# Kernel tuning notes

Hardware: AMD Instinct MI355X
Metric: run time of the kernel (lower is better)

## Reference

```python
import jax, jax.numpy as jnp
import numpy as np

N = 100000   # nodes (users+objects merged into one table)
M = 32768    # interactions (edges)
D = 256      # emb_dim == inter_dim
E = 2        # etypes: trusts, rates


def setup_inputs() -> dict:
    key = jax.random.key(0)
    ks = jax.random.split(key, 24)
    s = 1.0 / np.sqrt(D)
    f = lambda k, shp: (jax.random.normal(k, shp, dtype=jnp.float32) * s)
    return {
        "src": jax.random.randint(ks[0], (M,), 0, N),
        "dst": jax.random.randint(ks[1], (M,), 0, N),
        "etype": jax.random.randint(ks[2], (M,), 0, E),
        "dt": jax.random.uniform(ks[3], (M,), dtype=jnp.float32),
        "hid": f(ks[4], (N, D)),
        "cell": f(ks[5], (N, D)),
        # per-etype relation MLPs (source side and target side), layer==1 -> Lin-ReLU-Lin
        "W1s": f(ks[6], (E, D, D)), "b1s": f(ks[7], (E, D)),
        "W2s": f(ks[8], (E, D, D)), "b2s": f(ks[9], (E, D)),
        "W1g": f(ks[10], (E, D, D)), "b1g": f(ks[11], (E, D)),
        "W2g": f(ks[12], (E, D, D)), "b2g": f(ks[13], (E, D)),
        # attention combine (p, q, linear_s, linear_g)
        "p_w": f(ks[14], (D,)), "p_b": jnp.zeros((), jnp.float32),
        "q_w": f(ks[15], (D,)), "q_b": jnp.zeros((), jnp.float32),
        "Ws_w": f(ks[16], (D, D)), "Ws_b": f(ks[17], (D,)),
        "Wg_w": f(ks[18], (D, D)), "Wg_b": f(ks[19], (D,)),
        # time-aware LSTM cell (TLSTMCell(inter_dim=D, emb_dim=D))
        "Wx": f(ks[20], (D, 4 * D)), "Wh": f(ks[21], (D, 4 * D)),
        "b_lstm": jnp.zeros((4 * D,), jnp.float32),
        # final score head
        "w_out": f(ks[22], (D,)), "b_out": jnp.zeros((), jnp.float32),
        "decay_w": jnp.float32(0.1),
    }


def _rel_mlp(x, W1, b1, W2, b2, onehot):
    # x: [M,D]; W1,W2: [E,D,D]; dispatch through per-etype MLP, select by etype.
    h = jax.nn.relu(jnp.einsum('md,edk->emk', x, W1) + b1[:, None, :])   # [E,M,D]
    y = jnp.einsum('emd,edk->emk', h, W2) + b2[:, None, :]               # [E,M,D]
    return jnp.einsum('emd,me->md', y, onehot)                            # [M,D]


def reference(src, dst, etype, dt, hid, cell,
              W1s, b1s, W2s, b2s, W1g, b1g, W2g, b2g,
              p_w, p_b, q_w, q_b, Ws_w, Ws_b, Wg_w, Wg_b,
              Wx, Wh, b_lstm, w_out, b_out, decay_w):
    onehot = jax.nn.one_hot(etype, E, dtype=hid.dtype)  # [M,E]
    h_s = hid[src]   # [M,D] source hidden
    h_g = hid[dst]   # [M,D] target hidden
    c_g = cell[dst]  # [M,D] target cell

    # relation-specific MLPs (RelationNN)
    msg_s = _rel_mlp(h_s, W1s, b1s, W2s, b2s, onehot)
    msg_g = _rel_mlp(h_g, W1g, b1g, W2g, b2g, onehot)

    # attention-gated interaction combine (p/q + linear_s/linear_g)
    a = jax.nn.sigmoid(msg_s @ p_w + p_b + msg_g @ q_w + q_b)[:, None]  # [M,1]
    x = a * (msg_s @ Ws_w.T + Ws_b) + (1.0 - a) * (msg_g @ Wg_w.T + Wg_b)

    # time decay of target cell state (Decay, exp method)
    c_dec = c_g * jnp.exp(-jnp.abs(decay_w) * dt)[:, None]

    # TLSTM cell update for target node
    gates = x @ Wx + h_g @ Wh + b_lstm                                    # [M,4D]
    i_g, f_g, g_g, o_g = jnp.split(gates, 4, axis=-1)
    c_new = jax.nn.sigmoid(f_g) * c_dec + jax.nn.sigmoid(i_g) * jnp.tanh(g_g)
    h_new = jax.nn.sigmoid(o_g) * jnp.tanh(c_new)

    # edge score head (linear -> sigmoid)
    score = jax.nn.sigmoid(h_new @ w_out + b_out)                         # [M]
    return score, h_new, c_new
```

## Files before the change

kernel.cpp:

```cpp
#include <hip/hip_runtime.h>


#define M_EDGES 32768
#define S_TOP   32896
#define GRID_U  257

typedef __bf16 bf16_t;
typedef __bf16 bf16x8 __attribute__((ext_vector_type(8)));
typedef float  f32x4  __attribute__((ext_vector_type(4)));

#define OFF_W1ST 0
#define OFF_W2ST 131072
#define OFF_W1GT 262144
#define OFF_W2GT 393216
#define OFF_WST  524288
#define OFF_WGT  589824
#define OFF_WXT  655360
#define OFF_WHT  917504
#define WBUF_ELEMS 1179648

__device__ __forceinline__ float sigm_f(float x) { return 1.f / (1.f + __expf(-x)); }
__device__ __forceinline__ float tanh_f(float x) {
  x = fminf(fmaxf(x, -15.f), 15.f);
  float e = __expf(2.f * x);
  return (e - 1.f) / (e + 1.f);
}
__device__ __forceinline__ unsigned short* swzp(unsigned short* base, int n, int byteoff) {
  return (unsigned short*)((char*)base + (byteoff ^ ((((n >> 3) ^ n) & 7) << 4)));
}

__global__ __launch_bounds__(256)
void k_init(const float* __restrict__ W1s, const float* __restrict__ W2s,
            const float* __restrict__ W1g, const float* __restrict__ W2g,
            const float* __restrict__ Wsw, const float* __restrict__ Wgw,
            const float* __restrict__ Wx,  const float* __restrict__ Wh,
            bf16_t* __restrict__ wbuf, int* __restrict__ eid,
            int* __restrict__ srcn, int* __restrict__ dstn,
            float* __restrict__ dts, int* __restrict__ cnt)
{
  const int b = blockIdx.x, tid = threadIdx.x;
  if (b < 256) {
    const float* src; bf16_t* dst; int C_in, n0, k0;
    if (b < 128) {
      const int grp = b >> 5, e = (b >> 4) & 1, t16 = b & 15;
      const float* bases[4] = {W1s, W2s, W1g, W2g};
      src = bases[grp] + e * 65536;
      dst = wbuf + grp * 131072 + e * 65536;
      C_in = 256; n0 = (t16 >> 2) * 64; k0 = (t16 & 3) * 64;
    } else {
      const int b2 = b - 128, mat = b2 >> 6, t64 = b2 & 63;
      src = mat ? Wh : Wx;
      dst = wbuf + OFF_WXT + mat * 262144;
      C_in = 1024; n0 = (t64 >> 2) * 64; k0 = (t64 & 3) * 64;
    }
    __shared__ float tile[64][65];
    const int r = tid >> 2, cg = (tid & 3) * 16;
#pragma unroll
    for (int j = 0; j < 4; ++j) {
      float4 v = *(const float4*)(src + (k0 + r) * C_in + n0 + cg + 4 * j);
      tile[r][cg + 4 * j + 0] = v.x;
      tile[r][cg + 4 * j + 1] = v.y;
      tile[r][cg + 4 * j + 2] = v.z;
      tile[r][cg + 4 * j + 3] = v.w;
    }
    __syncthreads();
    const int c2 = tid >> 2, rg = (tid & 3) * 16;
#pragma unroll
    for (int j = 0; j < 16; ++j)
      dst[(n0 + c2) * 256 + k0 + rg + j] = (bf16_t)tile[rg + j][c2];
  } else {
    const int idx0 = (b - 256) * 256 + tid;
    for (int i = idx0; i < 65536; i += 32768) {
      wbuf[OFF_WST + i] = (bf16_t)Wsw[i];
      wbuf[OFF_WGT + i] = (bf16_t)Wgw[i];
    }
    for (int i = idx0; i < S_TOP; i += 32768) {
      eid[i] = -1; srcn[i] = 0; dstn[i] = 0; dts[i] = 0.f;
    }
    if (idx0 < 2) cnt[idx0] = 0;
  }
}

__global__ __launch_bounds__(256)
void k_slots(const int* __restrict__ etype, const int* __restrict__ src,
             const int* __restrict__ dst, const float* __restrict__ dt,
             int* __restrict__ cnt, int* __restrict__ eid, int* __restrict__ srcn,
             int* __restrict__ dstn, float* __restrict__ dts)
{
  const int m = blockIdx.x * 256 + threadIdx.x;
  const int lane = threadIdx.x & 63;
  const int e = etype[m];
  const unsigned long long b0 = __ballot(e == 0);
  const unsigned long long lt = (1ull << lane) - 1;
  const int c0 = __popcll(b0);
  int a0 = 0, a1 = 0;
  if (lane == 0) {
    a0 = atomicAdd(&cnt[0], c0);
    a1 = atomicAdd(&cnt[1], 64 - c0);
  }
  a0 = __shfl(a0, 0);
  a1 = __shfl(a1, 0);
  const int pos = (e == 0) ? (a0 + __popcll(b0 & lt))
                           : (a1 + __popcll(~b0 & lt));
  const int s = (e == 0) ? pos : (S_TOP - 1 - pos);
  eid[s] = m; srcn[s] = src[m]; dstn[s] = dst[m]; dts[s] = dt[m];
}

__global__ __launch_bounds__(256)
void k_gather(const float* __restrict__ hid, const int* __restrict__ srcn,
              const int* __restrict__ dstn, bf16_t* __restrict__ Xs,
              bf16_t* __restrict__ Xg)
{
  const int s = blockIdx.x * 4 + (threadIdx.x >> 6);
  const int c = (threadIdx.x & 63) * 4;
  const int ns = srcn[s], ng = dstn[s];
  float4 vs = *(const float4*)(hid + (size_t)ns * 256 + c);
  float4 vg = *(const float4*)(hid + (size_t)ng * 256 + c);
  union { bf16_t h[4]; unsigned long long u; } pk;
  pk.h[0] = (bf16_t)vs.x; pk.h[1] = (bf16_t)vs.y; pk.h[2] = (bf16_t)vs.z; pk.h[3] = (bf16_t)vs.w;
  *(unsigned long long*)(Xs + s * 256 + c) = pk.u;
  pk.h[0] = (bf16_t)vg.x; pk.h[1] = (bf16_t)vg.y; pk.h[2] = (bf16_t)vg.z; pk.h[3] = (bf16_t)vg.w;
  *(unsigned long long*)(Xg + s * 256 + c) = pk.u;
}

template<int EPI, bool DUAL>
__global__ __launch_bounds__(256, 2)
void k_gemm(const bf16_t* __restrict__ A, const bf16_t* __restrict__ A2,
            const bf16_t* __restrict__ W0, const bf16_t* __restrict__ W1,
            const bf16_t* __restrict__ W20, const bf16_t* __restrict__ W21,
            const float* __restrict__ bias0, const float* __restrict__ bias1,
            bf16_t* __restrict__ Out, const int* __restrict__ cnt,
            const float* __restrict__ pq, float* __restrict__ ps,
            float* __restrict__ aarr, const float* __restrict__ sb0,
            const float* __restrict__ sb1, const bf16_t* __restrict__ Tmat)
{
  const int tid = threadIdx.x;
  const int w = tid >> 6, lane = tid & 63, lo = lane & 15, hi = lane >> 4;
  const int row0 = blockIdx.x * 128;
  const int cnt0 = cnt[0], cnt1 = cnt[1];
  const int cnt0r = (cnt0 + 127) & ~127;
  const int v1 = S_TOP - cnt1;
  if (row0 >= cnt0r && row0 + 128 <= v1) return;
  const int e = (row0 < cnt0r) ? 0 : 1;
  const float* bias = e ? bias1 : bias0;

  __shared__ unsigned short Bt[256 * 64];
  __shared__ float sdot[128];

  f32x4 acc[8][4];
  const f32x4 z4 = {0.f, 0.f, 0.f, 0.f};
#pragma unroll
  for (int rb = 0; rb < 8; ++rb)
#pragma unroll
    for (int tc = 0; tc < 4; ++tc) acc[rb][tc] = z4;

  const int nph = DUAL ? 2 : 1;
  for (int ph = 0; ph < nph; ++ph) {
    const bf16_t* Ap = (DUAL && ph) ? A2 : A;
    const bf16_t* Wp = (DUAL && ph) ? (e ? W21 : W20) : (e ? W1 : W0);
    for (int c = 0; c < 4; ++c) {
      __syncthreads();
#pragma unroll
      for (int p = 0; p < 4; ++p) {
        const int n = (tid >> 2) + p * 64;
        const int i0 = tid & 3;
        const bf16_t* sp = Wp + n * 256 + c * 64;
        bf16x8 v0 = *(const bf16x8*)(sp + i0 * 8);
        bf16x8 v1 = *(const bf16x8*)(sp + 32 + i0 * 8);
        *(bf16x8*)swzp(Bt, n, n * 128 + i0 * 16) = v0;
        *(bf16x8*)swzp(Bt, n, n * 128 + 64 + i0 * 16) = v1;
      }
      __syncthreads();
#pragma unroll
      for (int ks = 0; ks < 2; ++ks) {
        bf16x8 af[8];
#pragma unroll
        for (int rb = 0; rb < 8; ++rb)
          af[rb] = *(const bf16x8*)(Ap + (row0 + rb * 16 + lo) * 256 + c * 64 + ks * 32 + hi * 8);
#pragma unroll
        for (int tc = 0; tc < 4; ++tc) {
          const int n = w * 64 + tc * 16 + lo;
          bf16x8 bf = *(const bf16x8*)swzp(Bt, n, n * 128 + ks * 64 + hi * 16);
#pragma unroll
          for (int rb = 0; rb < 8; ++rb)
            acc[rb][tc] = __builtin_amdgcn_mfma_f32_16x16x32_bf16(af[rb], bf, acc[rb][tc], 0, 0, 0);
        }
      }
    }
  }

  if (EPI == 1 || EPI == 2) {
    if (tid < 128) sdot[tid] = 0.f;
    __syncthreads();
  }

  float dots[8][4];
#pragma unroll
  for (int rb = 0; rb < 8; ++rb)
#pragma unroll
    for (int i = 0; i < 4; ++i) dots[rb][i] = 0.f;

#pragma unroll
  for (int rb = 0; rb < 8; ++rb) {
#pragma unroll
    for (int tc = 0; tc < 4; ++tc) {
      const int col = w * 64 + tc * 16 + lo;
      const float bs = bias[col];
      const float pqv = (EPI == 1 || EPI == 2) ? pq[col] : 0.f;
      f32x4 v = acc[rb][tc];
#pragma unroll
      for (int i = 0; i < 4; ++i) {
        const int row = row0 + rb * 16 + hi * 4 + i;
        float val = v[i] + bs;
        if (EPI == 0) val = fmaxf(val, 0.f);
        if (EPI == 4) {
          const float av = aarr[row];
          const float tv = (float)Tmat[row * 256 + col];
          val = av * tv + (1.f - av) * val;
        }
        if (EPI == 1 || EPI == 2) dots[rb][i] += val * pqv;
        Out[row * 256 + col] = (bf16_t)val;
      }
    }
  }

  if (EPI == 1 || EPI == 2) {
#pragma unroll
    for (int rb = 0; rb < 8; ++rb) {
#pragma unroll
      for (int i = 0; i < 4; ++i) {
        float d = dots[rb][i];
        d += __shfl_xor(d, 1); d += __shfl_xor(d, 2);
        d += __shfl_xor(d, 4); d += __shfl_xor(d, 8);
        if (lo == 0) atomicAdd(&sdot[rb * 16 + hi * 4 + i], d);
      }
    }
    __syncthreads();
    if (tid < 128) {
      const int row = row0 + tid;
      if (EPI == 1) ps[row] = sdot[tid];
      else          aarr[row] = sigm_f(ps[row] + sdot[tid] + sb0[0] + sb1[0]);
    }
  }
}

__global__ __launch_bounds__(256)
void k_lstm(const bf16_t* __restrict__ Gi, const bf16_t* __restrict__ Gf,
            const bf16_t* __restrict__ Gg, const bf16_t* __restrict__ Go,
            const float* __restrict__ cell, const int* __restrict__ eid,
            const int* __restrict__ dstn, const float* __restrict__ dts,
            const float* __restrict__ w_out, const float* __restrict__ b_out,
            const float* __restrict__ decay_w,
            float* __restrict__ outS, float* __restrict__ outH, float* __restrict__ outC)
{
  const int s = blockIdx.x * 4 + (threadIdx.x >> 6);
  const int lane = threadIdx.x & 63;
  const int m = eid[s];
  const int nd = dstn[s];
  const float dec = __expf(-fabsf(decay_w[0]) * dts[s]);
  float part = 0.f;
#pragma unroll
  for (int j = 0; j < 4; ++j) {
    const int cdim = j * 64 + lane;
    const float iv = (float)Gi[s * 256 + cdim];
    const float fv = (float)Gf[s * 256 + cdim];
    const float gv = (float)Gg[s * 256 + cdim];
    const float ov = (float)Go[s * 256 + cdim];
    const float cg = cell[(size_t)nd * 256 + cdim];
    const float cn = sigm_f(fv) * (cg * dec) + sigm_f(iv) * tanh_f(gv);
    const float hn = sigm_f(ov) * tanh_f(cn);
    if (m >= 0) {
      outH[(size_t)m * 256 + cdim] = hn;
      outC[(size_t)m * 256 + cdim] = cn;
    }
    part += hn * w_out[cdim];
  }
#pragma unroll
  for (int msk = 1; msk < 64; msk <<= 1) part += __shfl_xor(part, msk);
  if (lane == 0 && m >= 0) outS[m] = sigm_f(part + b_out[0]);
}

extern "C" void kernel_launch(void* const* d_in, const int* in_sizes, int n_in,
                              void* d_out, int out_size, void* d_ws, size_t ws_size,
                              hipStream_t stream)
{
  const int*   src     = (const int*)d_in[0];
  const int*   dst     = (const int*)d_in[1];
  const int*   etype   = (const int*)d_in[2];
  const float* dt      = (const float*)d_in[3];
  const float* hid     = (const float*)d_in[4];
  const float* cell    = (const float*)d_in[5];
  const float* W1s     = (const float*)d_in[6];
  const float* b1s     = (const float*)d_in[7];
  const float* W2s     = (const float*)d_in[8];
  const float* b2s     = (const float*)d_in[9];
  const float* W1g     = (const float*)d_in[10];
  const float* b1g     = (const float*)d_in[11];
  const float* W2g     = (const float*)d_in[12];
  const float* b2g     = (const float*)d_in[13];
  const float* p_w     = (const float*)d_in[14];
  const float* p_b     = (const float*)d_in[15];
  const float* q_w     = (const float*)d_in[16];
  const float* q_b     = (const float*)d_in[17];
  const float* Ws_w    = (const float*)d_in[18];
  const float* Ws_b    = (const float*)d_in[19];
  const float* Wg_w    = (const float*)d_in[20];
  const float* Wg_b    = (const float*)d_in[21];
  const float* Wx      = (const float*)d_in[22];
  const float* Wh      = (const float*)d_in[23];
  const float* b_lstm  = (const float*)d_in[24];
  const float* w_out   = (const float*)d_in[25];
  const float* b_out   = (const float*)d_in[26];
  const float* decay_w = (const float*)d_in[27];
  (void)in_sizes; (void)n_in; (void)out_size; (void)ws_size;

  char* p = (char*)d_ws;
  auto alloc = [&](size_t bytes) { char* r = p; p += (bytes + 255) & ~(size_t)255; return r; };
  const size_t SB = (size_t)S_TOP * 256 * sizeof(bf16_t);
  bf16_t* wbuf = (bf16_t*)alloc(WBUF_ELEMS * sizeof(bf16_t));
  bf16_t* Xs   = (bf16_t*)alloc(SB);
  bf16_t* Xg   = (bf16_t*)alloc(SB);
  bf16_t* B1   = (bf16_t*)alloc(SB);
  bf16_t* B2   = (bf16_t*)alloc(SB);
  bf16_t* B3   = (bf16_t*)alloc(SB);
  bf16_t* B4   = (bf16_t*)alloc(SB);
  float*  psb  = (float*)alloc(S_TOP * 4);
  float*  aarr = (float*)alloc(S_TOP * 4);
  int*    eid  = (int*)alloc(S_TOP * 4);
  int*    srcn = (int*)alloc(S_TOP * 4);
  int*    dstn = (int*)alloc(S_TOP * 4);
  float*  dts  = (float*)alloc(S_TOP * 4);
  int*    cnt  = (int*)alloc(256);

  float* outS = (float*)d_out;
  float* outH = outS + M_EDGES;
  float* outC = outH + (size_t)M_EDGES * 256;

  k_init<<<384, 256, 0, stream>>>(W1s, W2s, W1g, W2g, Ws_w, Wg_w, Wx, Wh,
                                  wbuf, eid, srcn, dstn, dts, cnt);
  k_slots<<<M_EDGES / 256, 256, 0, stream>>>(etype, src, dst, dt, cnt, eid, srcn, dstn, dts);
  k_gather<<<S_TOP / 4, 256, 0, stream>>>(hid, srcn, dstn, Xs, Xg);

  k_gemm<0, false><<<GRID_U, 256, 0, stream>>>(Xs, nullptr,
      wbuf + OFF_W1ST, wbuf + OFF_W1ST + 65536, nullptr, nullptr,
      b1s, b1s + 256, B1, cnt, nullptr, nullptr, nullptr, nullptr, nullptr, nullptr);
  k_gemm<1, false><<<GRID_U, 256, 0, stream>>>(B1, nullptr,
      wbuf + OFF_W2ST, wbuf + OFF_W2ST + 65536, nullptr, nullptr,
      b2s, b2s + 256, B2, cnt, p_w, psb, nullptr, nullptr, nullptr, nullptr);
  k_gemm<0, false><<<GRID_U, 256, 0, stream>>>(Xg, nullptr,
      wbuf + OFF_W1GT, wbuf + OFF_W1GT + 65536, nullptr, nullptr,
      b1g, b1g + 256, B1, cnt, nullptr, nullptr, nullptr, nullptr, nullptr, nullptr);
  k_gemm<2, false><<<GRID_U, 256, 0, stream>>>(B1, nullptr,
      wbuf + OFF_W2GT, wbuf + OFF_W2GT + 65536, nullptr, nullptr,
      b2g, b2g + 256, B3, cnt, q_w, psb, aarr, p_b, q_b, nullptr);
  k_gemm<3, false><<<GRID_U, 256, 0, stream>>>(B2, nullptr,
      wbuf + OFF_WST, wbuf + OFF_WST, nullptr, nullptr,
      Ws_b, Ws_b, B1, cnt, nullptr, nullptr, nullptr, nullptr, nullptr, nullptr);
  k_gemm<4, false><<<GRID_U, 256, 0, stream>>>(B3, nullptr,
      wbuf + OFF_WGT, wbuf + OFF_WGT, nullptr, nullptr,
      Wg_b, Wg_b, B4, cnt, nullptr, nullptr, aarr, nullptr, nullptr, B1);
  bf16_t* gbuf[4] = {Xs, B1, B2, B3};
  for (int g = 0; g < 4; ++g) {
    k_gemm<3, true><<<GRID_U, 256, 0, stream>>>(B4, Xg,
        wbuf + OFF_WXT + g * 65536, wbuf + OFF_WXT + g * 65536,
        wbuf + OFF_WHT + g * 65536, wbuf + OFF_WHT + g * 65536,
        b_lstm + g * 256, b_lstm + g * 256, gbuf[g], cnt,
        nullptr, nullptr, nullptr, nullptr, nullptr, nullptr);
  }
  k_lstm<<<S_TOP / 4, 256, 0, stream>>>(gbuf[0], gbuf[1], gbuf[2], gbuf[3],
      cell, eid, dstn, dts, w_out, b_out, decay_w, outS, outH, outC);
}
```

Before: 618.3 us.

## Fuse all relation MLP, attention and LSTM GEMMs into one megakernel

Replaces the chain of ten GEMM launches and the separate LSTM kernel with a single kernel. Each block processes 64 edge rows end to end, keeping intermediate activations in LDS and registers instead of round-tripping bf16 buffers through global memory. Weights are now read directly from global memory (L2) per MFMA fragment rather than staged in LDS. The trade-off is more register pressure (accumulators, the T buffer and the carry state live at the same time), smaller row tiles, and possibly lower occupancy.

```diff
diff --git a/kernel.cpp b/kernel.cpp
--- a/kernel.cpp
+++ b/kernel.cpp
@@ -3,7 +3,8 @@
 
 #define M_EDGES 32768
 #define S_TOP   32896
-#define GRID_U  257
+#define TROWS   64
+#define GRID_MEGA (S_TOP / TROWS)
 
 typedef __bf16 bf16_t;
 typedef __bf16 bf16x8 __attribute__((ext_vector_type(8)));
@@ -24,9 +25,6 @@
   x = fminf(fmaxf(x, -15.f), 15.f);
   float e = __expf(2.f * x);
   return (e - 1.f) / (e + 1.f);
-}
-__device__ __forceinline__ unsigned short* swzp(unsigned short* base, int n, int byteoff) {
-  return (unsigned short*)((char*)base + (byteoff ^ ((((n >> 3) ^ n) & 7) << 4)));
 }
 
 __global__ __launch_bounds__(256)
@@ -123,161 +121,292 @@
   *(unsigned long long*)(Xg + s * 256 + c) = pk.u;
 }
 
-template<int EPI, bool DUAL>
+__device__ __forceinline__ bf16x8 gfrag(const bf16_t* b, int row, int k) {
+  return *(const bf16x8*)(b + (size_t)row * 256 + k);
+}
+__device__ __forceinline__ bf16x8 lfrag(const unsigned short* buf, int row, int kbyte) {
+  return *(const bf16x8*)((const char*)buf + row * 512 + (kbyte ^ ((row & 7) << 4)));
+}
+__device__ __forceinline__ void lstore(unsigned short* buf, int row, int colbyte, bf16_t v) {
+  *(bf16_t*)((char*)buf + row * 512 + (colbyte ^ ((row & 7) << 4))) = v;
+}
+__device__ __forceinline__ void zacc(f32x4 (&acc)[4][4]) {
+  const f32x4 z = {0.f, 0.f, 0.f, 0.f};
+#pragma unroll
+  for (int a = 0; a < 4; ++a)
+#pragma unroll
+    for (int b = 0; b < 4; ++b) acc[a][b] = z;
+}
+template<bool LDSA>
+__device__ __forceinline__ void gacc(f32x4 (&acc)[4][4], const unsigned short* lb,
+                                     const bf16_t* gA, int grow0,
+                                     const bf16_t* W, int w, int lo, int hi)
+{
+#pragma unroll
+  for (int c = 0; c < 4; ++c)
+#pragma unroll
+    for (int ks = 0; ks < 2; ++ks) {
+      const int k = c * 64 + ks * 32 + hi * 8;
+      bf16x8 af[4];
+#pragma unroll
+      for (int rb = 0; rb < 4; ++rb) {
+        if constexpr (LDSA) af[rb] = lfrag(lb, rb * 16 + lo, k * 2);
+        else                af[rb] = gfrag(gA, grow0 + rb * 16 + lo, k);
+      }
+#pragma unroll
+      for (int tc = 0; tc < 4; ++tc) {
+        bf16x8 bfv = gfrag(W, w * 64 + tc * 16 + lo, k);
+#pragma unroll
+        for (int rb = 0; rb < 4; ++rb)
+          acc[rb][tc] = __builtin_amdgcn_mfma_f32_16x16x32_bf16(af[rb], bfv, acc[rb][tc], 0, 0, 0);
+      }
+    }
+}
+
 __global__ __launch_bounds__(256, 2)
-void k_gemm(const bf16_t* __restrict__ A, const bf16_t* __restrict__ A2,
-            const bf16_t* __restrict__ W0, const bf16_t* __restrict__ W1,
-            const bf16_t* __restrict__ W20, const bf16_t* __restrict__ W21,
-            const float* __restrict__ bias0, const float* __restrict__ bias1,
-            bf16_t* __restrict__ Out, const int* __restrict__ cnt,
-            const float* __restrict__ pq, float* __restrict__ ps,
-            float* __restrict__ aarr, const float* __restrict__ sb0,
-            const float* __restrict__ sb1, const bf16_t* __restrict__ Tmat)
+void k_mega(const bf16_t* __restrict__ Xs, const bf16_t* __restrict__ Xg,
+            const bf16_t* __restrict__ wbuf,
+            const float* __restrict__ b1s, const float* __restrict__ b2s,
+            const float* __restrict__ b1g, const float* __restrict__ b2g,
+            const float* __restrict__ p_w, const float* __restrict__ p_b,
+            const float* __restrict__ q_w, const float* __restrict__ q_b,
+            const float* __restrict__ Wsb, const float* __restrict__ Wgb,
+            const float* __restrict__ b_lstm, const float* __restrict__ w_out,
+            const float* __restrict__ b_out, const float* __restrict__ decay_w,
+            const float* __restrict__ cell, const int* __restrict__ cnt,
+            const int* __restrict__ eid, const int* __restrict__ dstn,
+            const float* __restrict__ dts,
+            float* __restrict__ outS, float* __restrict__ outH, float* __restrict__ outC)
 {
   const int tid = threadIdx.x;
   const int w = tid >> 6, lane = tid & 63, lo = lane & 15, hi = lane >> 4;
-  const int row0 = blockIdx.x * 128;
+  const int row0 = blockIdx.x * TROWS;
   const int cnt0 = cnt[0], cnt1 = cnt[1];
-  const int cnt0r = (cnt0 + 127) & ~127;
+  const int cnt0r = (cnt0 + TROWS - 1) & ~(TROWS - 1);
   const int v1 = S_TOP - cnt1;
-  if (row0 >= cnt0r && row0 + 128 <= v1) return;
+  if (row0 >= cnt0r && row0 + TROWS <= v1) return;
   const int e = (row0 < cnt0r) ? 0 : 1;
-  const float* bias = e ? bias1 : bias0;
-
-  __shared__ unsigned short Bt[256 * 64];
-  __shared__ float sdot[128];
-
-  f32x4 acc[8][4];
-  const f32x4 z4 = {0.f, 0.f, 0.f, 0.f};
-#pragma unroll
-  for (int rb = 0; rb < 8; ++rb)
-#pragma unroll
-    for (int tc = 0; tc < 4; ++tc) acc[rb][tc] = z4;
-
-  const int nph = DUAL ? 2 : 1;
-  for (int ph = 0; ph < nph; ++ph) {
-    const bf16_t* Ap = (DUAL && ph) ? A2 : A;
-    const bf16_t* Wp = (DUAL && ph) ? (e ? W21 : W20) : (e ? W1 : W0);
-    for (int c = 0; c < 4; ++c) {
-      __syncthreads();
-#pragma unroll
-      for (int p = 0; p < 4; ++p) {
-        const int n = (tid >> 2) + p * 64;
-        const int i0 = tid & 3;
-        const bf16_t* sp = Wp + n * 256 + c * 64;
-        bf16x8 v0 = *(const bf16x8*)(sp + i0 * 8);
-        bf16x8 v1 = *(const bf16x8*)(sp + 32 + i0 * 8);
-        *(bf16x8*)swzp(Bt, n, n * 128 + i0 * 16) = v0;
-        *(bf16x8*)swzp(Bt, n, n * 128 + 64 + i0 * 16) = v1;
-      }
-      __syncthreads();
-#pragma unroll
-      for (int ks = 0; ks < 2; ++ks) {
-        bf16x8 af[8];
-#pragma unroll
-        for (int rb = 0; rb < 8; ++rb)
-          af[rb] = *(const bf16x8*)(Ap + (row0 + rb * 16 + lo) * 256 + c * 64 + ks * 32 + hi * 8);
-#pragma unroll
-        for (int tc = 0; tc < 4; ++tc) {
-          const int n = w * 64 + tc * 16 + lo;
-          bf16x8 bf = *(const bf16x8*)swzp(Bt, n, n * 128 + ks * 64 + hi * 16);
-#pragma unroll
-          for (int rb = 0; rb < 8; ++rb)
-            acc[rb][tc] = __builtin_amdgcn_mfma_f32_16x16x32_bf16(af[rb], bf, acc[rb][tc], 0, 0, 0);
-        }
-      }
-    }
-  }
-
-  if (EPI == 1 || EPI == 2) {
-    if (tid < 128) sdot[tid] = 0.f;
-    __syncthreads();
-  }
-
-  float dots[8][4];
-#pragma unroll
-  for (int rb = 0; rb < 8; ++rb)
-#pragma unroll
-    for (int i = 0; i < 4; ++i) dots[rb][i] = 0.f;
-
-#pragma unroll
-  for (int rb = 0; rb < 8; ++rb) {
+
+  __shared__ unsigned short bufA[TROWS * 256];
+  __shared__ unsigned short bufB[TROWS * 256];
+  __shared__ float ps[TROWS], qs[TROWS], aa[TROWS], sdot[TROWS], decv[TROWS];
+  __shared__ int leid[TROWS], lnd[TROWS];
+
+  if (tid < TROWS) {
+    const int r = row0 + tid;
+    ps[tid] = 0.f; qs[tid] = 0.f; sdot[tid] = 0.f;
+    leid[tid] = eid[r]; lnd[tid] = dstn[r];
+    decv[tid] = __expf(-fabsf(decay_w[0]) * dts[r]);
+  }
+
+  f32x4 acc[4][4];
+
+  zacc(acc);
+  gacc<false>(acc, nullptr, Xs, row0, wbuf + OFF_W1ST + e * 65536, w, lo, hi);
+  {
+    const float* bias = b1s + e * 256;
 #pragma unroll
     for (int tc = 0; tc < 4; ++tc) {
       const int col = w * 64 + tc * 16 + lo;
       const float bs = bias[col];
-      const float pqv = (EPI == 1 || EPI == 2) ? pq[col] : 0.f;
-      f32x4 v = acc[rb][tc];
+#pragma unroll
+      for (int rb = 0; rb < 4; ++rb)
+#pragma unroll
+        for (int i = 0; i < 4; ++i)
+          lstore(bufA, rb * 16 + hi * 4 + i, col * 2, (bf16_t)fmaxf(acc[rb][tc][i] + bs, 0.f));
+    }
+  }
+  __syncthreads();
+
+  zacc(acc);
+  gacc<true>(acc, bufA, nullptr, 0, wbuf + OFF_W2ST + e * 65536, w, lo, hi);
+  {
+    const float* bias = b2s + e * 256;
+    float dp[4][4] = {};
+#pragma unroll
+    for (int tc = 0; tc < 4; ++tc) {
+      const int col = w * 64 + tc * 16 + lo;
+      const float bs = bias[col], pw = p_w[col];
+#pragma unroll
+      for (int rb = 0; rb < 4; ++rb)
+#pragma unroll
+        for (int i = 0; i < 4; ++i) {
+          const float v = acc[rb][tc][i] + bs;
+          lstore(bufB, rb * 16 + hi * 4 + i, col * 2, (bf16_t)v);
+          dp[rb][i] += v * pw;
+        }
+    }
+#pragma unroll
+    for (int rb = 0; rb < 4; ++rb)
 #pragma unroll
       for (int i = 0; i < 4; ++i) {
-        const int row = row0 + rb * 16 + hi * 4 + i;
-        float val = v[i] + bs;
-        if (EPI == 0) val = fmaxf(val, 0.f);
-        if (EPI == 4) {
-          const float av = aarr[row];
-          const float tv = (float)Tmat[row * 256 + col];
-          val = av * tv + (1.f - av) * val;
+        float d = dp[rb][i];
+        d += __shfl_xor(d, 1); d += __shfl_xor(d, 2);
+        d += __shfl_xor(d, 4); d += __shfl_xor(d, 8);
+        if (lo == 0) atomicAdd(&ps[rb * 16 + hi * 4 + i], d);
+      }
+  }
+  __syncthreads();
+
+  f32x4 T[4][4];
+  zacc(acc);
+  gacc<true>(acc, bufB, nullptr, 0, wbuf + OFF_WST, w, lo, hi);
+#pragma unroll
+  for (int tc = 0; tc < 4; ++tc) {
+    const float bs = Wsb[w * 64 + tc * 16 + lo];
+#pragma unroll
+    for (int rb = 0; rb < 4; ++rb)
+#pragma unroll
+      for (int i = 0; i < 4; ++i) T[rb][tc][i] = acc[rb][tc][i] + bs;
+  }
+
+  zacc(acc);
+  gacc<false>(acc, nullptr, Xg, row0, wbuf + OFF_W1GT + e * 65536, w, lo, hi);
+  {
+    const float* bias = b1g + e * 256;
+#pragma unroll
+    for (int tc = 0; tc < 4; ++tc) {
+      const int col = w * 64 + tc * 16 + lo;
+      const float bs = bias[col];
+#pragma unroll
+      for (int rb = 0; rb < 4; ++rb)
+#pragma unroll
+        for (int i = 0; i < 4; ++i)
+          lstore(bufA, rb * 16 + hi * 4 + i, col * 2, (bf16_t)fmaxf(acc[rb][tc][i] + bs, 0.f));
+    }
+  }
+  __syncthreads();
+
+  zacc(acc);
+  gacc<true>(acc, bufA, nullptr, 0, wbuf + OFF_W2GT + e * 65536, w, lo, hi);
+  {
+    const float* bias = b2g + e * 256;
+    float dp[4][4] = {};
+#pragma unroll
+    for (int tc = 0; tc < 4; ++tc) {
+      const int col = w * 64 + tc * 16 + lo;
+      const float bs = bias[col], qw = q_w[col];
+#pragma unroll
+      for (int rb = 0; rb < 4; ++rb)
+#pragma unroll
+        for (int i = 0; i < 4; ++i) {
+          const float v = acc[rb][tc][i] + bs;
+          lstore(bufB, rb * 16 + hi * 4 + i, col * 2, (bf16_t)v);
+          dp[rb][i] += v * qw;
         }
-        if (EPI == 1 || EPI == 2) dots[rb][i] += val * pqv;
-        Out[row * 256 + col] = (bf16_t)val;
-      }
-    }
-  }
-
-  if (EPI == 1 || EPI == 2) {
-#pragma unroll
-    for (int rb = 0; rb < 8; ++rb) {
+    }
+#pragma unroll
+    for (int rb = 0; rb < 4; ++rb)
 #pragma unroll
       for (int i = 0; i < 4; ++i) {
-        float d = dots[rb][i];
+        float d = dp[rb][i];
+        d += __shfl_xor(d, 1); d += __shfl_xor(d, 2);
+        d += __shfl_xor(d, 4); d += __shfl_xor(d, 8);
+        if (lo == 0) atomicAdd(&qs[rb * 16 + hi * 4 + i], d);
+      }
+  }
+  __syncthreads();
+
+  if (tid < TROWS) aa[tid] = sigm_f(ps[tid] + qs[tid] + p_b[0] + q_b[0]);
+  __syncthreads();
+
+  zacc(acc);
+  gacc<true>(acc, bufB, nullptr, 0, wbuf + OFF_WGT, w, lo, hi);
+#pragma unroll
+  for (int tc = 0; tc < 4; ++tc) {
+    const int col = w * 64 + tc * 16 + lo;
+    const float bs = Wgb[col];
+#pragma unroll
+    for (int rb = 0; rb < 4; ++rb)
+#pragma unroll
+      for (int i = 0; i < 4; ++i) {
+        const int ri = rb * 16 + hi * 4 + i;
+        const float av = aa[ri];
+        const float x = av * T[rb][tc][i] + (1.f - av) * (acc[rb][tc][i] + bs);
+        lstore(bufA, ri, col * 2, (bf16_t)x);
+      }
+  }
+  __syncthreads();
+
+  f32x4 carry[4][4];
+  zacc(acc);
+  gacc<true >(acc, bufA, nullptr, 0, wbuf + OFF_WXT + 2 * 65536, w, lo, hi);
+  gacc<false>(acc, nullptr, Xg, row0, wbuf + OFF_WHT + 2 * 65536, w, lo, hi);
+#pragma unroll
+  for (int tc = 0; tc < 4; ++tc) {
+    const float bs = b_lstm[2 * 256 + w * 64 + tc * 16 + lo];
+#pragma unroll
+    for (int rb = 0; rb < 4; ++rb)
+#pragma unroll
+      for (int i = 0; i < 4; ++i) carry[rb][tc][i] = tanh_f(acc[rb][tc][i] + bs);
+  }
+  zacc(acc);
+  gacc<true >(acc, bufA, nullptr, 0, wbuf + OFF_WXT + 0 * 65536, w, lo, hi);
+  gacc<false>(acc, nullptr, Xg, row0, wbuf + OFF_WHT + 0 * 65536, w, lo, hi);
+#pragma unroll
+  for (int tc = 0; tc < 4; ++tc) {
+    const float bs = b_lstm[0 * 256 + w * 64 + tc * 16 + lo];
+#pragma unroll
+    for (int rb = 0; rb < 4; ++rb)
+#pragma unroll
+      for (int i = 0; i < 4; ++i) carry[rb][tc][i] *= sigm_f(acc[rb][tc][i] + bs);
+  }
+  zacc(acc);
+  gacc<true >(acc, bufA, nullptr, 0, wbuf + OFF_WXT + 1 * 65536, w, lo, hi);
+  gacc<false>(acc, nullptr, Xg, row0, wbuf + OFF_WHT + 1 * 65536, w, lo, hi);
+#pragma unroll
+  for (int tc = 0; tc < 4; ++tc) {
+    const int col = w * 64 + tc * 16 + lo;
+    const float bs = b_lstm[1 * 256 + col];
+#pragma unroll
+    for (int rb = 0; rb < 4; ++rb)
+#pragma unroll
+      for (int i = 0; i < 4; ++i) {
+        const int ri = rb * 16 + hi * 4 + i;
+        const float cdec = cell[(size_t)lnd[ri] * 256 + col] * decv[ri];
+        carry[rb][tc][i] += sigm_f(acc[rb][tc][i] + bs) * cdec;
+      }
+  }
+  zacc(acc);
+  gacc<true >(acc, bufA, nullptr, 0, wbuf + OFF_WXT + 3 * 65536, w, lo, hi);
+  gacc<false>(acc, nullptr, Xg, row0, wbuf + OFF_WHT + 3 * 65536, w, lo, hi);
+  {
+    float dp[4][4] = {};
+#pragma unroll
+    for (int tc = 0; tc < 4; ++tc) {
+      const int col = w * 64 + tc * 16 + lo;
+      const float bs = b_lstm[3 * 256 + col];
+      const float wo = w_out[col];
+#pragma unroll
+      for (int rb = 0; rb < 4; ++rb)
+#pragma unroll
+        for (int i = 0; i < 4; ++i) {
+          const int ri = rb * 16 + hi * 4 + i;
+          const int m = leid[ri];
+          const float cn = carry[rb][tc][i];
+          const float hn = sigm_f(acc[rb][tc][i] + bs) * tanh_f(cn);
+          if (m >= 0) {
+            outH[(size_t)m * 256 + col] = hn;
+            outC[(size_t)m * 256 + col] = cn;
+          }
+          dp[rb][i] += hn * wo;
+        }
+    }
+#pragma unroll
+    for (int rb = 0; rb < 4; ++rb)
+#pragma unroll
+      for (int i = 0; i < 4; ++i) {
+        float d = dp[rb][i];
         d += __shfl_xor(d, 1); d += __shfl_xor(d, 2);
         d += __shfl_xor(d, 4); d += __shfl_xor(d, 8);
         if (lo == 0) atomicAdd(&sdot[rb * 16 + hi * 4 + i], d);
       }
-    }
-    __syncthreads();
-    if (tid < 128) {
-      const int row = row0 + tid;
-      if (EPI == 1) ps[row] = sdot[tid];
-      else          aarr[row] = sigm_f(ps[row] + sdot[tid] + sb0[0] + sb1[0]);
-    }
-  }
-}
-
-__global__ __launch_bounds__(256)
-void k_lstm(const bf16_t* __restrict__ Gi, const bf16_t* __restrict__ Gf,
-            const bf16_t* __restrict__ Gg, const bf16_t* __restrict__ Go,
-            const float* __restrict__ cell, const int* __restrict__ eid,
-            const int* __restrict__ dstn, const float* __restrict__ dts,
-            const float* __restrict__ w_out, const float* __restrict__ b_out,
-            const float* __restrict__ decay_w,
-            float* __restrict__ outS, float* __restrict__ outH, float* __restrict__ outC)
-{
-  const int s = blockIdx.x * 4 + (threadIdx.x >> 6);
-  const int lane = threadIdx.x & 63;
-  const int m = eid[s];
-  const int nd = dstn[s];
-  const float dec = __expf(-fabsf(decay_w[0]) * dts[s]);
-  float part = 0.f;
-#pragma unroll
-  for (int j = 0; j < 4; ++j) {
-    const int cdim = j * 64 + lane;
-    const float iv = (float)Gi[s * 256 + cdim];
-    const float fv = (float)Gf[s * 256 + cdim];
-    const float gv = (float)Gg[s * 256 + cdim];
-    const float ov = (float)Go[s * 256 + cdim];
-    const float cg = cell[(size_t)nd * 256 + cdim];
-    const float cn = sigm_f(fv) * (cg * dec) + sigm_f(iv) * tanh_f(gv);
-    const float hn = sigm_f(ov) * tanh_f(cn);
-    if (m >= 0) {
-      outH[(size_t)m * 256 + cdim] = hn;
-      outC[(size_t)m * 256 + cdim] = cn;
-    }
-    part += hn * w_out[cdim];
-  }
-#pragma unroll
-  for (int msk = 1; msk < 64; msk <<= 1) part += __shfl_xor(part, msk);
-  if (lane == 0 && m >= 0) outS[m] = sigm_f(part + b_out[0]);
+  }
+  __syncthreads();
+  if (tid < TROWS) {
+    const int m = leid[tid];
+    if (m >= 0) outS[m] = sigm_f(sdot[tid] + b_out[0]);
+  }
 }
 
 extern "C" void kernel_launch(void* const* d_in, const int* in_sizes, int n_in,
@@ -320,12 +449,6 @@
   bf16_t* wbuf = (bf16_t*)alloc(WBUF_ELEMS * sizeof(bf16_t));
   bf16_t* Xs   = (bf16_t*)alloc(SB);
   bf16_t* Xg   = (bf16_t*)alloc(SB);
-  bf16_t* B1   = (bf16_t*)alloc(SB);
-  bf16_t* B2   = (bf16_t*)alloc(SB);
-  bf16_t* B3   = (bf16_t*)alloc(SB);
-  bf16_t* B4   = (bf16_t*)alloc(SB);
-  float*  psb  = (float*)alloc(S_TOP * 4);
-  float*  aarr = (float*)alloc(S_TOP * 4);
   int*    eid  = (int*)alloc(S_TOP * 4);
   int*    srcn = (int*)alloc(S_TOP * 4);
   int*    dstn = (int*)alloc(S_TOP * 4);
@@ -340,33 +463,8 @@
                                   wbuf, eid, srcn, dstn, dts, cnt);
   k_slots<<<M_EDGES / 256, 256, 0, stream>>>(etype, src, dst, dt, cnt, eid, srcn, dstn, dts);
   k_gather<<<S_TOP / 4, 256, 0, stream>>>(hid, srcn, dstn, Xs, Xg);
-
-  k_gemm<0, false><<<GRID_U, 256, 0, stream>>>(Xs, nullptr,
-      wbuf + OFF_W1ST, wbuf + OFF_W1ST + 65536, nullptr, nullptr,
-      b1s, b1s + 256, B1, cnt, nullptr, nullptr, nullptr, nullptr, nullptr, nullptr);
-  k_gemm<1, false><<<GRID_U, 256, 0, stream>>>(B1, nullptr,
-      wbuf + OFF_W2ST, wbuf + OFF_W2ST + 65536, nullptr, nullptr,
-      b2s, b2s + 256, B2, cnt, p_w, psb, nullptr, nullptr, nullptr, nullptr);
-  k_gemm<0, false><<<GRID_U, 256, 0, stream>>>(Xg, nullptr,
-      wbuf + OFF_W1GT, wbuf + OFF_W1GT + 65536, nullptr, nullptr,
-      b1g, b1g + 256, B1, cnt, nullptr, nullptr, nullptr, nullptr, nullptr, nullptr);
-  k_gemm<2, false><<<GRID_U, 256, 0, stream>>>(B1, nullptr,
-      wbuf + OFF_W2GT, wbuf + OFF_W2GT + 65536, nullptr, nullptr,
-      b2g, b2g + 256, B3, cnt, q_w, psb, aarr, p_b, q_b, nullptr);
-  k_gemm<3, false><<<GRID_U, 256, 0, stream>>>(B2, nullptr,
-      wbuf + OFF_WST, wbuf + OFF_WST, nullptr, nullptr,
-      Ws_b, Ws_b, B1, cnt, nullptr, nullptr, nullptr, nullptr, nullptr, nullptr);
-  k_gemm<4, false><<<GRID_U, 256, 0, stream>>>(B3, nullptr,
-      wbuf + OFF_WGT, wbuf + OFF_WGT, nullptr, nullptr,
-      Wg_b, Wg_b, B4, cnt, nullptr, nullptr, aarr, nullptr, nullptr, B1);
-  bf16_t* gbuf[4] = {Xs, B1, B2, B3};
-  for (int g = 0; g < 4; ++g) {
-    k_gemm<3, true><<<GRID_U, 256, 0, stream>>>(B4, Xg,
-        wbuf + OFF_WXT + g * 65536, wbuf + OFF_WXT + g * 65536,
-        wbuf + OFF_WHT + g * 65536, wbuf + OFF_WHT + g * 65536,
-        b_lstm + g * 256, b_lstm + g * 256, gbuf[g], cnt,
-        nullptr, nullptr, nullptr, nullptr, nullptr, nullptr);
-  }
-  k_lstm<<<S_TOP / 4, 256, 0, stream>>>(gbuf[0], gbuf[1], gbuf[2], gbuf[3],
-      cell, eid, dstn, dts, w_out, b_out, decay_w, outS, outH, outC);
-}
+  k_mega<<<GRID_MEGA, 256, 0, stream>>>(Xs, Xg, wbuf,
+      b1s, b2s, b1g, b2g, p_w, p_b, q_w, q_b, Ws_b, Wg_b,
+      b_lstm, w_out, b_out, decay_w, cell, cnt, eid, dstn, dts,
+      outS, outH, outC);
+}
```

Result: slower. 1.074 ms (+73.6%).
